# Performance work log

Hardware: AMD Instinct MI355X
Metric: run time of the kernel (lower is better)

The kernel has to match this reference:

```python
import jax, jax.numpy as jnp
import numpy as np

B, S, D, H = 2, 2048, 1024, 16
HD = D // H


def setup_inputs() -> dict:
    key = jax.random.key(0)
    ks = jax.random.split(key, 6)
    std = 1.0 / np.sqrt(D)
    return {
        "hidden_states": jax.random.normal(ks[0], (B, S, D), dtype=jnp.float32),
        "attention_mask": jnp.zeros((B, 1, S, S), dtype=jnp.float32),
        "Wq": jax.random.normal(ks[1], (D, D), dtype=jnp.float32) * std,
        "bq": jnp.zeros((D,), dtype=jnp.float32),
        "Wk": jax.random.normal(ks[2], (D, D), dtype=jnp.float32) * std,
        "bk": jnp.zeros((D,), dtype=jnp.float32),
        "Wv": jax.random.normal(ks[3], (D, D), dtype=jnp.float32) * std,
        "bv": jnp.zeros((D,), dtype=jnp.float32),
        "Wo": jax.random.normal(ks[4], (D, D), dtype=jnp.float32) * std,
        "bo": jnp.zeros((D,), dtype=jnp.float32),
    }


def reference(hidden_states, attention_mask, Wq, bq, Wk, bk, Wv, bv, Wo, bo):
    scale = HD ** (-0.5)
    # torch Linear: y = x @ W^T + b
    def proj(x, W, b):
        y = jnp.einsum('bsd,ed->bse', x, W) + b
        return y.reshape(B, S, H, HD).transpose(0, 2, 1, 3)  # [B,H,S,HD]
    q = proj(hidden_states, Wq, bq)
    k = proj(hidden_states, Wk, bk)
    v = proj(hidden_states, Wv, bv)
    scores = jnp.einsum('bhqd,bhkd->bhqk', q, k) * scale + attention_mask
    attn = jax.nn.softmax(scores, axis=-1)  # dropout p=0.0 -> identity
    out = jnp.einsum('bhqk,bhkd->bhqd', attn, v)
    out = out.transpose(0, 2, 1, 3).reshape(B, S, D)
    return jnp.einsum('bsd,ed->bse', out, Wo) + bo
```

## Files before the change

kernel.cpp:

```cpp
#include <hip/hip_runtime.h>
#include <hip/hip_bf16.h>
#include <stdint.h>

#define Bb 2
#define Ss 2048
#define Dd 1024
#define Hh 16
#define HD 64

typedef __attribute__((ext_vector_type(8))) __bf16 bf16x8;
typedef __attribute__((ext_vector_type(4))) __bf16 bf16x4;
typedef __attribute__((ext_vector_type(2))) __bf16 bf16x2;
typedef __attribute__((ext_vector_type(4))) float f32x4;
typedef __attribute__((ext_vector_type(16))) float f32x16;

#define LOG2E 1.44269504088896f
#define SCL2 (0.125f * LOG2E)

#define HS_N   (Bb * Ss * Dd)
#define W_N    (Dd * Dd)
#define B_N    (Dd)
#define CAN_HS 0
#define CAN_WQ (CAN_HS + HS_N)
#define CAN_BQ (CAN_WQ + W_N)
#define CAN_WK (CAN_BQ + B_N)
#define CAN_BK (CAN_WK + W_N)
#define CAN_WV (CAN_BK + B_N)
#define CAN_BV (CAN_WV + W_N)
#define CAN_WO (CAN_BV + B_N)
#define CAN_BO (CAN_WO + W_N)
#define CAN_END (CAN_BO + B_N)
#define TSZ    (Bb * Hh * Ss * HD)
#define WS_ELEMS (CAN_END + 4 * TSZ)
#define WS_NEED ((size_t)WS_ELEMS * 2)

__device__ __forceinline__ void gl_lds16(const __bf16* g, __bf16* l) {
  __builtin_amdgcn_global_load_lds(
      (const __attribute__((address_space(1))) void*)g,
      (__attribute__((address_space(3))) void*)l,
      16, 0, 0);
}

__device__ __forceinline__ void cfence() { asm volatile("" ::: "memory"); }

__global__ void canon_kernel(const float* hs, const float* Wq, const float* bq,
                             const float* Wk, const float* bk, const float* Wv,
                             const float* bv, const float* Wo, const float* bo,
                             __bf16* __restrict__ dst) {
  const float* srcs[9] = {hs, Wq, bq, Wk, bk, Wv, bv, Wo, bo};
  const long starts[10] = {CAN_HS, CAN_WQ, CAN_BQ, CAN_WK, CAN_BK,
                           CAN_WV, CAN_BV, CAN_WO, CAN_BO, CAN_END};
  const long nchunks = CAN_END / 8;
  for (long c = blockIdx.x * blockDim.x + threadIdx.x; c < nchunks;
       c += (long)gridDim.x * blockDim.x) {
    const long i = c * 8;
    int seg = 0;
#pragma unroll
    for (int t = 1; t < 9; t++) seg += (i >= starts[t]) ? 1 : 0;
    const float* s = srcs[seg] + (i - starts[seg]);
    bf16x8 v;
#pragma unroll
    for (int e = 0; e < 8; e++) v[e] = (__bf16)s[e];
    *(bf16x8*)(dst + i) = v;
  }
}

__global__ __launch_bounds__(256, 2) void gemm_qkv(
    const __bf16* __restrict__ A,
    const __bf16* __restrict__ W0, const __bf16* __restrict__ W1,
    const __bf16* __restrict__ W2,
    const __bf16* __restrict__ b0, const __bf16* __restrict__ b1,
    const __bf16* __restrict__ b2,
    __bf16* __restrict__ O0, __bf16* __restrict__ O1, __bf16* __restrict__ O2) {
  __shared__ __align__(16) __bf16 sA[128 * 32];
  __shared__ __align__(16) __bf16 sB[128 * 32];
  const int tid = threadIdx.x;
  const int lane = tid & 63;
  const int wid = tid >> 6;
  const int quad = lane >> 4;
  const int l15 = lane & 15;
  const int mBlock = blockIdx.x * 128;

  const int which = blockIdx.y >> 3;
  const int nBlock = (blockIdx.y & 7) * 128;
  const __bf16* W = which == 0 ? W0 : (which == 1 ? W1 : W2);
  const __bf16* bias = which == 0 ? b0 : (which == 1 ? b1 : b2);
  __bf16* Out = which == 0 ? O0 : (which == 1 ? O1 : O2);

  const int waveM = (wid >> 1) * 64;
  const int waveN = (wid & 1) * 64;

  f32x4 acc[4][4] = {};

  const int c1 = wid * 64 + lane;
  const int c2 = c1 + 256;
  const __bf16* Ar1 = A + (mBlock + (c1 >> 2)) * Dd + (c1 & 3) * 8;
  const __bf16* Ar2 = A + (mBlock + (c2 >> 2)) * Dd + (c2 & 3) * 8;
  const __bf16* Wr1 = W + (nBlock + (c1 >> 2)) * Dd + (c1 & 3) * 8;
  const __bf16* Wr2 = W + (nBlock + (c2 >> 2)) * Dd + (c2 & 3) * 8;
  __bf16* ldsA1 = sA + c1 * 8;
  __bf16* ldsA2 = sA + c2 * 8;
  __bf16* ldsB1 = sB + c1 * 8;
  __bf16* ldsB2 = sB + c2 * 8;

  for (int k0 = 0; k0 < Dd; k0 += 32) {
    gl_lds16(Ar1 + k0, ldsA1);
    gl_lds16(Ar2 + k0, ldsA2);
    gl_lds16(Wr1 + k0, ldsB1);
    gl_lds16(Wr2 + k0, ldsB2);
    __syncthreads();

    bf16x8 aF[4], bF[4];
#pragma unroll
    for (int mi = 0; mi < 4; mi++)
      aF[mi] = *(const bf16x8*)(sA + (waveM + mi * 16 + l15) * 32 + quad * 8);
#pragma unroll
    for (int ni = 0; ni < 4; ni++)
      bF[ni] = *(const bf16x8*)(sB + (waveN + ni * 16 + l15) * 32 + quad * 8);
#pragma unroll
    for (int mi = 0; mi < 4; mi++)
#pragma unroll
      for (int ni = 0; ni < 4; ni++)
        acc[mi][ni] = __builtin_amdgcn_mfma_f32_16x16x32_bf16(
            aF[mi], bF[ni], acc[mi][ni], 0, 0, 0);
    __syncthreads();
  }

#pragma unroll
  for (int ni = 0; ni < 4; ni++) {
    const int ng = nBlock + waveN + ni * 16 + l15;
    const float bv = (float)bias[ng];
#pragma unroll
    for (int mi = 0; mi < 4; mi++) {
      const int mg0 = mBlock + waveM + mi * 16 + quad * 4;
      if (which == 2) {
        const int b = mg0 >> 11, s0 = mg0 & 2047;
        const int h = ng >> 6, hd = ng & 63;
        bf16x4 pk;
#pragma unroll
        for (int r = 0; r < 4; r++) pk[r] = (__bf16)(acc[mi][ni][r] + bv);
        *(bf16x4*)(Out + (((b * Hh + h) * HD + hd) * Ss) + s0) = pk;
      } else {
#pragma unroll
        for (int r = 0; r < 4; r++) {
          float v = acc[mi][ni][r] + bv;
          if (which == 0) v *= SCL2;
          const int m = mg0 + r;
          const int b = m >> 11, s = m & 2047;
          const int h = ng >> 6, hd = ng & 63;
          Out[(((b * Hh + h) * Ss + s) * HD) + hd] = (__bf16)v;
        }
      }
    }
  }
}

__global__ __launch_bounds__(256, 2) void gemm_out(
    const __bf16* __restrict__ A, const __bf16* __restrict__ W,
    const __bf16* __restrict__ bias, float* __restrict__ Out) {
  __shared__ __align__(16) __bf16 sA[2][128][32];
  __shared__ __align__(16) __bf16 sB[2][64][32];
  const int tid = threadIdx.x;
  const int lane = tid & 63;
  const int wid = tid >> 6;
  const int quad = lane >> 4;
  const int l15 = lane & 15;
  const int mBlock = blockIdx.x * 128;
  const int nBlock = blockIdx.y * 64;

  const int waveM = (wid >> 1) * 64;
  const int waveN = (wid & 1) * 32;

  f32x4 acc[4][2] = {};

  for (int k0 = 0; k0 < Dd; k0 += 64) {
#pragma unroll
    for (int j = 0; j < 4; j++) {
      const int c = j * 256 + tid;
      gl_lds16(A + (mBlock + ((c >> 2) & 127)) * Dd + k0 + (c >> 9) * 32 +
                   (c & 3) * 8,
               &sA[0][0][0] + c * 8);
    }
#pragma unroll
    for (int j = 0; j < 2; j++) {
      const int c = j * 256 + tid;
      gl_lds16(W + (nBlock + ((c >> 2) & 63)) * Dd + k0 + (c >> 8) * 32 +
                   (c & 3) * 8,
               &sB[0][0][0] + c * 8);
    }
    __syncthreads();

#pragma unroll
    for (int ks = 0; ks < 2; ks++) {
      bf16x8 aF[4], bF[2];
#pragma unroll
      for (int mi = 0; mi < 4; mi++)
        aF[mi] = *(const bf16x8*)&sA[ks][waveM + mi * 16 + l15][quad * 8];
#pragma unroll
      for (int ni = 0; ni < 2; ni++)
        bF[ni] = *(const bf16x8*)&sB[ks][waveN + ni * 16 + l15][quad * 8];
#pragma unroll
      for (int mi = 0; mi < 4; mi++)
#pragma unroll
        for (int ni = 0; ni < 2; ni++)
          acc[mi][ni] = __builtin_amdgcn_mfma_f32_16x16x32_bf16(
              aF[mi], bF[ni], acc[mi][ni], 0, 0, 0);
    }
    __syncthreads();
  }

#pragma unroll
  for (int ni = 0; ni < 2; ni++) {
    const int ng = nBlock + waveN + ni * 16 + l15;
    const float bv = (float)bias[ng];
#pragma unroll
    for (int mi = 0; mi < 4; mi++) {
      const int mg0 = mBlock + waveM + mi * 16 + quad * 4;
#pragma unroll
      for (int r = 0; r < 4; r++)
        Out[(mg0 + r) * Dd + ng] = acc[mi][ni][r] + bv;
    }
  }
}

__global__ __launch_bounds__(256, 4) void attn_fused(
    const __bf16* __restrict__ Qg, const __bf16* __restrict__ Kg,
    const __bf16* __restrict__ Vt, const float* __restrict__ Mf,
    __bf16* __restrict__ Og) {
  __shared__ __align__(16) union {
    __bf16 buf[2][8192];
    struct {
      float O[2][64][32];
      float L[2][32];
    } m;
  } sh;

  const int tid = threadIdx.x;
  const int lane = tid & 63;
  const int wid = tid >> 6;
  const int qg = wid & 1;
  const int kvh = wid >> 1;
  const int l31 = lane & 31;
  const int hi = lane >> 5;
  const int bh = blockIdx.y;
  const int b = bh >> 4;
  const int h = bh & 15;
  const int qw = blockIdx.x * 64 + qg * 32 + l31;

  const __bf16* Qp = Qg + (size_t)bh * Ss * HD;
  const __bf16* Kp = Kg + (size_t)bh * Ss * HD;
  const __bf16* Vp = Vt + (size_t)bh * HD * Ss;
  const float* Mrow = Mf + ((size_t)b * Ss + qw) * Ss + 32 * kvh + 4 * hi;

  bf16x8 qf[4];
#pragma unroll
  for (int k = 0; k < 4; k++)
    qf[k] = *(const bf16x8*)(Qp + (size_t)qw * HD + k * 16 + hi * 8);

  const int cA = tid, cB = 256 + tid;
#define STAGE_KV(BI, KVS)                                                     \
  {                                                                           \
    __bf16* kb = sh.buf[BI];                                                  \
    gl_lds16(Kp + ((KVS) + ((cA >> 1) & 63)) * HD + (cA >> 7) * 16 +          \
                 (cA & 1) * 8, kb + cA * 8);                                  \
    gl_lds16(Kp + ((KVS) + ((cB >> 1) & 63)) * HD + (cB >> 7) * 16 +          \
                 (cB & 1) * 8, kb + cB * 8);                                  \
    __bf16* vb = sh.buf[BI] + 4096;                                           \
    gl_lds16(Vp + (size_t)((cA >> 1) & 63) * Ss + (KVS) + (cA >> 7) * 16 +    \
                 (cA & 1) * 8, vb + cA * 8);                                  \
    gl_lds16(Vp + (size_t)((cB >> 1) & 63) * Ss + (KVS) + (cB >> 7) * 16 +    \
                 (cB & 1) * 8, vb + cB * 8);                                  \
  }

  f32x16 o[2] = {};
  f32x4 lacc = {0.f, 0.f, 0.f, 0.f};

  STAGE_KV(0, 0);

  for (int it = 0; it < 32; ++it) {
    const int kv0 = it * 64;
    const int bufc = it & 1;
    cfence();
    __builtin_amdgcn_s_barrier();
    cfence();
    f32x4 mc[4];
#pragma unroll
    for (int g = 0; g < 4; g++) mc[g] = *(const f32x4*)(Mrow + kv0 + g * 8);
    cfence();
    if (it < 31) {
      STAGE_KV(bufc ^ 1, kv0 + 64);
      cfence();
      asm volatile("s_waitcnt vmcnt(8)" ::: "memory");
    } else {
      asm volatile("s_waitcnt vmcnt(4)" ::: "memory");
    }
    __builtin_amdgcn_s_barrier();
    cfence();

    f32x16 sacc = {};
#pragma unroll
    for (int k = 0; k < 4; k++) {
      bf16x8 kf = *(const bf16x8*)(sh.buf[bufc] + k * 1024 +
                                   (kvh * 32 + l31) * 16 + hi * 8);
      sacc = __builtin_amdgcn_mfma_f32_32x32x16_bf16(kf, qf[k], sacc, 0, 0, 0);
    }

    f32x4 sv[4];
#pragma unroll
    for (int g = 0; g < 4; g++)
#pragma unroll
      for (int r = 0; r < 4; r++)
        sv[g][r] = __builtin_amdgcn_exp2f(sacc[g * 4 + r] + mc[g][r] * LOG2E);
    lacc += (sv[0] + sv[1]) + (sv[2] + sv[3]);

    bf16x4 pk[4];
#pragma unroll
    for (int g = 0; g < 4; g++)
#pragma unroll
      for (int r = 0; r < 4; r++) pk[g][r] = (__bf16)sv[g][r];
    union pu { bf16x4 v; uint32_t w[2]; };
    pu s0, s1, r0, r1;
    s0.v = hi ? pk[0] : pk[1];
    s1.v = hi ? pk[2] : pk[3];
    r0.w[0] = __shfl_xor((int)s0.w[0], 32);
    r0.w[1] = __shfl_xor((int)s0.w[1], 32);
    r1.w[0] = __shfl_xor((int)s1.w[0], 32);
    r1.w[1] = __shfl_xor((int)s1.w[1], 32);
    bf16x8 pf[2];
    {
      bf16x4 lo0 = hi ? r0.v : pk[0], hi0 = hi ? pk[1] : r0.v;
      bf16x4 lo1 = hi ? r1.v : pk[2], hi1 = hi ? pk[3] : r1.v;
#pragma unroll
      for (int e = 0; e < 4; e++) {
        pf[0][e] = lo0[e]; pf[0][e + 4] = hi0[e];
        pf[1][e] = lo1[e]; pf[1][e + 4] = hi1[e];
      }
    }

#pragma unroll
    for (int k = 0; k < 2; k++)
#pragma unroll
      for (int hb = 0; hb < 2; hb++) {
        bf16x8 vf = *(const bf16x8*)(sh.buf[bufc] + 4096 +
                                     (kvh * 2 + k) * 1024 +
                                     (hb * 32 + l31) * 16 + hi * 8);
        o[hb] = __builtin_amdgcn_mfma_f32_32x32x16_bf16(vf, pf[k], o[hb],
                                                        0, 0, 0);
      }
  }

  float l = lacc[0] + lacc[1] + lacc[2] + lacc[3];
  l += __shfl_xor(l, 32);

  __syncthreads();
  if (kvh == 1) {
#pragma unroll
    for (int hb = 0; hb < 2; hb++)
#pragma unroll
      for (int r = 0; r < 16; r++) {
        const int hd = hb * 32 + (r & 3) + 8 * (r >> 2) + 4 * hi;
        sh.m.O[qg][hd][l31] = o[hb][r];
      }
    if (hi == 0) sh.m.L[qg][l31] = l;
  }
  __syncthreads();
  if (kvh == 0) {
#pragma unroll
    for (int hb = 0; hb < 2; hb++)
#pragma unroll
      for (int r = 0; r < 16; r++) {
        const int hd = hb * 32 + (r & 3) + 8 * (r >> 2) + 4 * hi;
        o[hb][r] += sh.m.O[qg][hd][l31];
      }
    l += sh.m.L[qg][l31];
    const float inv = 1.0f / l;
    __bf16* Ow = Og + (((size_t)b * Ss + qw) * Hh + h) * HD;
#pragma unroll
    for (int hb = 0; hb < 2; hb++)
#pragma unroll
      for (int g = 0; g < 4; g++) {
        const int hd = hb * 32 + g * 8 + 4 * hi;
        bf16x2 w0, w1;
        w0[0] = (__bf16)(o[hb][g * 4 + 0] * inv);
        w0[1] = (__bf16)(o[hb][g * 4 + 1] * inv);
        w1[0] = (__bf16)(o[hb][g * 4 + 2] * inv);
        w1[1] = (__bf16)(o[hb][g * 4 + 3] * inv);
        *(bf16x2*)(Ow + hd) = w0;
        *(bf16x2*)(Ow + hd + 2) = w1;
      }
  }
}

extern "C" void kernel_launch(void* const* d_in, const int* in_sizes, int n_in,
                              void* d_out, int out_size, void* d_ws,
                              size_t ws_size, hipStream_t stream) {
  if (ws_size < WS_NEED) return;

  __bf16* ws = (__bf16*)d_ws;
  const __bf16* hsC = ws + CAN_HS;
  const __bf16* WqC = ws + CAN_WQ;
  const __bf16* bqC = ws + CAN_BQ;
  const __bf16* WkC = ws + CAN_WK;
  const __bf16* bkC = ws + CAN_BK;
  const __bf16* WvC = ws + CAN_WV;
  const __bf16* bvC = ws + CAN_BV;
  const __bf16* WoC = ws + CAN_WO;
  const __bf16* boC = ws + CAN_BO;
  __bf16* Q = ws + CAN_END;
  __bf16* K = Q + TSZ;
  __bf16* V = K + TSZ;
  __bf16* AW = V + TSZ;
  float* out = (float*)d_out;

  canon_kernel<<<2048, 256, 0, stream>>>(
      (const float*)d_in[0], (const float*)d_in[2], (const float*)d_in[3],
      (const float*)d_in[4], (const float*)d_in[5], (const float*)d_in[6],
      (const float*)d_in[7], (const float*)d_in[8], (const float*)d_in[9], ws);
  gemm_qkv<<<dim3(32, 24), 256, 0, stream>>>(hsC, WqC, WkC, WvC, bqC, bkC,
                                             bvC, Q, K, V);
  attn_fused<<<dim3(32, 32), 256, 0, stream>>>(Q, K, V, (const float*)d_in[1],
                                               AW);
  gemm_out<<<dim3(32, 16), 256, 0, stream>>>(AW, WoC, boC, out);
}
```

Baseline: 261.4 us.

## Shrink attention blocks to one query group and drop KV double buffering

```diff
diff --git a/kernel.cpp b/kernel.cpp
--- a/kernel.cpp
+++ b/kernel.cpp
@@ -41,8 +41,6 @@
       16, 0, 0);
 }
 
-__device__ __forceinline__ void cfence() { asm volatile("" ::: "memory"); }
-
 __global__ void canon_kernel(const float* hs, const float* Wq, const float* bq,
                              const float* Wk, const float* bk, const float* Wv,
                              const float* bv, const float* Wo, const float* bo,
@@ -65,7 +63,7 @@
   }
 }
 
-__global__ __launch_bounds__(256, 2) void gemm_qkv(
+__global__ __launch_bounds__(256, 3) void gemm_qkv(
     const __bf16* __restrict__ A,
     const __bf16* __restrict__ W0, const __bf16* __restrict__ W1,
     const __bf16* __restrict__ W2,
@@ -223,29 +221,27 @@
   }
 }
 
-__global__ __launch_bounds__(256, 4) void attn_fused(
+__global__ __launch_bounds__(128, 4) void attn_fused(
     const __bf16* __restrict__ Qg, const __bf16* __restrict__ Kg,
     const __bf16* __restrict__ Vt, const float* __restrict__ Mf,
     __bf16* __restrict__ Og) {
   __shared__ __align__(16) union {
-    __bf16 buf[2][8192];
+    __bf16 buf[8192];
     struct {
-      float O[2][64][32];
-      float L[2][32];
+      float O[64][32];
+      float L[32];
     } m;
   } sh;
 
   const int tid = threadIdx.x;
   const int lane = tid & 63;
-  const int wid = tid >> 6;
-  const int qg = wid & 1;
-  const int kvh = wid >> 1;
+  const int kvh = tid >> 6;
   const int l31 = lane & 31;
   const int hi = lane >> 5;
   const int bh = blockIdx.y;
   const int b = bh >> 4;
   const int h = bh & 15;
-  const int qw = blockIdx.x * 64 + qg * 32 + l31;
+  const int qw = blockIdx.x * 32 + l31;
 
   const __bf16* Qp = Qg + (size_t)bh * Ss * HD;
   const __bf16* Kp = Kg + (size_t)bh * Ss * HD;
@@ -257,50 +253,34 @@
   for (int k = 0; k < 4; k++)
     qf[k] = *(const bf16x8*)(Qp + (size_t)qw * HD + k * 16 + hi * 8);
 
-  const int cA = tid, cB = 256 + tid;
-#define STAGE_KV(BI, KVS)                                                     \
-  {                                                                           \
-    __bf16* kb = sh.buf[BI];                                                  \
-    gl_lds16(Kp + ((KVS) + ((cA >> 1) & 63)) * HD + (cA >> 7) * 16 +          \
-                 (cA & 1) * 8, kb + cA * 8);                                  \
-    gl_lds16(Kp + ((KVS) + ((cB >> 1) & 63)) * HD + (cB >> 7) * 16 +          \
-                 (cB & 1) * 8, kb + cB * 8);                                  \
-    __bf16* vb = sh.buf[BI] + 4096;                                           \
-    gl_lds16(Vp + (size_t)((cA >> 1) & 63) * Ss + (KVS) + (cA >> 7) * 16 +    \
-                 (cA & 1) * 8, vb + cA * 8);                                  \
-    gl_lds16(Vp + (size_t)((cB >> 1) & 63) * Ss + (KVS) + (cB >> 7) * 16 +    \
-                 (cB & 1) * 8, vb + cB * 8);                                  \
-  }
-
   f32x16 o[2] = {};
   f32x4 lacc = {0.f, 0.f, 0.f, 0.f};
 
-  STAGE_KV(0, 0);
-
   for (int it = 0; it < 32; ++it) {
     const int kv0 = it * 64;
-    const int bufc = it & 1;
-    cfence();
-    __builtin_amdgcn_s_barrier();
-    cfence();
     f32x4 mc[4];
 #pragma unroll
     for (int g = 0; g < 4; g++) mc[g] = *(const f32x4*)(Mrow + kv0 + g * 8);
-    cfence();
-    if (it < 31) {
-      STAGE_KV(bufc ^ 1, kv0 + 64);
-      cfence();
-      asm volatile("s_waitcnt vmcnt(8)" ::: "memory");
-    } else {
-      asm volatile("s_waitcnt vmcnt(4)" ::: "memory");
-    }
-    __builtin_amdgcn_s_barrier();
-    cfence();
+
+#pragma unroll
+    for (int j = 0; j < 4; j++) {
+      const int c = j * 128 + tid;
+      gl_lds16(Kp + (kv0 + ((c >> 1) & 63)) * HD + (c >> 7) * 16 + (c & 1) * 8,
+               sh.buf + c * 8);
+    }
+#pragma unroll
+    for (int j = 0; j < 4; j++) {
+      const int c = j * 128 + tid;
+      gl_lds16(Vp + (size_t)((c >> 1) & 63) * Ss + kv0 + (c >> 7) * 16 +
+                   (c & 1) * 8,
+               sh.buf + 4096 + c * 8);
+    }
+    __syncthreads();
 
     f32x16 sacc = {};
 #pragma unroll
     for (int k = 0; k < 4; k++) {
-      bf16x8 kf = *(const bf16x8*)(sh.buf[bufc] + k * 1024 +
+      bf16x8 kf = *(const bf16x8*)(sh.buf + k * 1024 +
                                    (kvh * 32 + l31) * 16 + hi * 8);
       sacc = __builtin_amdgcn_mfma_f32_32x32x16_bf16(kf, qf[k], sacc, 0, 0, 0);
     }
@@ -341,27 +321,26 @@
     for (int k = 0; k < 2; k++)
 #pragma unroll
       for (int hb = 0; hb < 2; hb++) {
-        bf16x8 vf = *(const bf16x8*)(sh.buf[bufc] + 4096 +
-                                     (kvh * 2 + k) * 1024 +
+        bf16x8 vf = *(const bf16x8*)(sh.buf + 4096 + (kvh * 2 + k) * 1024 +
                                      (hb * 32 + l31) * 16 + hi * 8);
         o[hb] = __builtin_amdgcn_mfma_f32_32x32x16_bf16(vf, pf[k], o[hb],
                                                         0, 0, 0);
       }
+    __syncthreads();
   }
 
   float l = lacc[0] + lacc[1] + lacc[2] + lacc[3];
   l += __shfl_xor(l, 32);
 
-  __syncthreads();
   if (kvh == 1) {
 #pragma unroll
     for (int hb = 0; hb < 2; hb++)
 #pragma unroll
       for (int r = 0; r < 16; r++) {
         const int hd = hb * 32 + (r & 3) + 8 * (r >> 2) + 4 * hi;
-        sh.m.O[qg][hd][l31] = o[hb][r];
-      }
-    if (hi == 0) sh.m.L[qg][l31] = l;
+        sh.m.O[hd][l31] = o[hb][r];
+      }
+    if (hi == 0) sh.m.L[l31] = l;
   }
   __syncthreads();
   if (kvh == 0) {
@@ -370,9 +349,9 @@
 #pragma unroll
       for (int r = 0; r < 16; r++) {
         const int hd = hb * 32 + (r & 3) + 8 * (r >> 2) + 4 * hi;
-        o[hb][r] += sh.m.O[qg][hd][l31];
-      }
-    l += sh.m.L[qg][l31];
+        o[hb][r] += sh.m.O[hd][l31];
+      }
+    l += sh.m.L[l31];
     const float inv = 1.0f / l;
     __bf16* Ow = Og + (((size_t)b * Ss + qw) * Hh + h) * HD;
 #pragma unroll
@@ -418,7 +397,7 @@
       (const float*)d_in[7], (const float*)d_in[8], (const float*)d_in[9], ws);
   gemm_qkv<<<dim3(32, 24), 256, 0, stream>>>(hsC, WqC, WkC, WvC, bqC, bkC,
                                              bvC, Q, K, V);
-  attn_fused<<<dim3(32, 32), 256, 0, stream>>>(Q, K, V, (const float*)d_in[1],
+  attn_fused<<<dim3(64, 32), 128, 0, stream>>>(Q, K, V, (const float*)d_in[1],
                                                AW);
   gemm_out<<<dim3(32, 16), 256, 0, stream>>>(AW, WoC, boC, out);
 }
```

Result: slower. 287.7 us (+10.0%).
